# Kernel optimization log

Hardware: AMD Instinct MI355X
Metric: run time of the kernel (lower is better)

The kernel has to match this reference:

```python
import jax, jax.numpy as jnp
import numpy as np

TIMESTEPS = 1000
DIFFUSION_SPEED = 0.01
B, N = 4, 2048
E = N * (N - 1) // 2  # strict lower-triangular entries per graph


def _build_Qt():
    # Qt[t-1] = [[1-f, f], [f, 1-f]],  f = 0.5*(1-(1-2s)^t), t = 1..T
    ts = jnp.arange(1, TIMESTEPS + 1, dtype=jnp.float32)
    flip = 0.5 * (1.0 - (1.0 - 2.0 * DIFFUSION_SPEED) ** ts)          # [T]
    row0 = jnp.stack([1.0 - flip, flip], axis=-1)                      # [T,2]
    row1 = jnp.stack([flip, 1.0 - flip], axis=-1)                      # [T,2]
    return jnp.stack([row0, row1], axis=1)                             # [T,2,2]


def setup_inputs() -> dict:
    key = jax.random.key(0)
    k1, k2, k3, k4 = jax.random.split(key, 4)
    adj_start = jax.random.randint(k1, (B, N, N), 0, 2, dtype=jnp.int32)
    t = jax.random.randint(k2, (B,), 0, TIMESTEPS, dtype=jnp.int32)
    u = jax.random.uniform(k3, (B, N, N), dtype=jnp.float32)
    q_approx = jax.random.normal(k4, (B, E), dtype=jnp.float32)
    return {"adj_start": adj_start, "t": t, "u": u, "q_approx": q_approx}


def reference(adj_start, t, u, q_approx):
    Qt = _build_Qt()                                                   # [T,2,2]
    # symmetrize raw adjacency into a binary undirected adjacency
    a = jnp.tril(adj_start, -1)
    adj0 = a + jnp.swapaxes(a, -1, -2)                                 # [B,N,N] in {0,1}

    b_idx = jnp.arange(B)[:, None, None]

    # ---- forward diffusion: sample x_t ~ Categorical(Qt[t][adj0]) ----
    probs = Qt[t][b_idx, adj0]                                         # [B,N,N,2]
    x_t = (u < probs[..., 1]).astype(adj0.dtype)                       # [B,N,N]

    # ---- backward diffusion: q(x_{t-1} | x_t, x_0) ----
    Q_likelihood = Qt[0]                                               # [2,2]
    Q_prior = Qt[t - 1]                                                # [B,2,2] (t=0 wraps, as in torch)
    Q_evidence = Qt[t]                                                 # [B,2,2]

    likelihood = Q_likelihood[x_t]                                     # [B,N,N,2]
    prior = Q_prior[b_idx, adj0]                                       # [B,N,N,2]
    evidence = Q_evidence[b_idx, adj0, x_t]                            # [B,N,N]
    q_backward = likelihood * prior / evidence[..., None]              # [B,N,N,2]

    ti, tj = np.tril_indices(N, -1)                                    # static indices
    q_target = q_backward[:, ti, tj, 1]                                # [B,E]

    # ---- BCE-with-logits loss (mean) ----
    x = q_approx
    loss = jnp.mean(jnp.maximum(x, 0.0) - x * q_target + jnp.log1p(jnp.exp(-jnp.abs(x))))
    return loss
```

## Files before the change

kernel.cpp:

```cpp
#include <hip/hip_runtime.h>
#include <math.h>

#define TIMESTEPS 1000
constexpr int Bc  = 4;
constexpr int Nc  = 2048;
constexpr int EcI = Nc * (Nc - 1) / 2;
constexpr int EG  = EcI / 4;

constexpr int BLKX    = 128;
constexpr int THREADS = 256;
constexpr int ITERS   = 8;
constexpr int ITERSTRIDE = BLKX * THREADS * 2;

typedef int   i4v __attribute__((ext_vector_type(4)));
typedef float f4v __attribute__((ext_vector_type(4)));

__device__ __forceinline__ int imin(int a, int b) { return a < b ? a : b; }

struct GData { i4v av; f4v uv; f4v qv; };

__device__ __forceinline__ GData issue_group(
    const int* __restrict__ adjb, const float* __restrict__ ub,
    const float* __restrict__ qb, int gc)
{
    GData d;
    const int e0 = gc << 2;
    const float sf = sqrtf((float)(8 * e0 + 1));
    int i = (int)((1.0f + sf) * 0.5f);
    if (i * (i - 1) / 2 > e0)  --i;
    if (i * (i + 1) / 2 <= e0) ++i;
    int jj = e0 - i * (i - 1) / 2;
    d.qv = *(const f4v*)(qb + e0);
    int ii = i;
    #pragma unroll
    for (int k = 0; k < 4; ++k) {
        const bool adv = (jj >= ii);
        ii += adv;
        jj = adv ? 0 : jj;
        const int base = (ii << 11) + jj;
        d.av[k] = adjb[base];
        d.uv[k] = ub[base];
        ++jj;
    }
    return d;
}

__device__ __forceinline__ float group_sum(const GData& d,
    float p0, float p1, float qt00, float qt01, float qt10, float qt11)
{
    float s = 0.0f;
    #pragma unroll
    for (int k = 0; k < 4; ++k) {
        const int   a0 = d.av[k];
        const float ps = a0 ? p1 : p0;
        const bool  x  = d.uv[k] < ps;
        const float t0 = x ? qt01 : qt00;
        const float t1 = x ? qt11 : qt10;
        const float qt = a0 ? t1 : t0;
        const float qq = d.qv[k];
        s += fmaxf(qq, 0.0f) - qq * qt + __logf(1.0f + __expf(-fabsf(qq)));
    }
    return s;
}

__global__ __launch_bounds__(256, 2) void diff_loss_kernel(
    const int* __restrict__ adj, const int* __restrict__ t,
    const float* __restrict__ u, const float* __restrict__ q,
    double* __restrict__ partials)
{
    const int b  = blockIdx.y;
    const int bx = blockIdx.x;
    const int tb = t[b];

    const float f_t   = 0.5f * (1.0f - powf(0.98f, (float)(tb + 1)));
    const int   tpe   = (tb == 0) ? TIMESTEPS : tb;
    const float f_p   = 0.5f * (1.0f - powf(0.98f, (float)tpe));
    const float f0    = 0.01f;
    const float omf_t = 1.0f - f_t;

    const float p0   = f_t;
    const float p1   = omf_t;
    const float qt00 = f0          * f_p          / omf_t;
    const float qt01 = (1.0f - f0) * f_p          / f_t;
    const float qt10 = f0          * (1.0f - f_p) / f_t;
    const float qt11 = (1.0f - f0) * (1.0f - f_p) / omf_t;

    const int*   adjb = adj + ((size_t)b << 22);
    const float* ub   = u   + ((size_t)b << 22);
    const float* qb   = q   + (size_t)b * EcI;

    const int gbase = bx * 512 + threadIdx.x;

    GData A0 = issue_group(adjb, ub, qb, gbase);
    GData B0 = issue_group(adjb, ub, qb, gbase + 256);
    GData A1 = issue_group(adjb, ub, qb, gbase + ITERSTRIDE);
    GData B1 = issue_group(adjb, ub, qb, gbase + ITERSTRIDE + 256);

    double acc = 0.0;

    #pragma unroll 1
    for (int k = 0; k < ITERS; ++k) {
        GData An = A1, Bn = B1;
        if (k + 2 < ITERS) {
            const int gk = gbase + (k + 2) * ITERSTRIDE;
            An = issue_group(adjb, ub, qb, gk);
            Bn = issue_group(adjb, ub, qb, imin(gk + 256, EG - 1));
        }

        const float sA = group_sum(A0, p0, p1, qt00, qt01, qt10, qt11);
        const float sB = group_sum(B0, p0, p1, qt00, qt01, qt10, qt11);
        const int g1 = gbase + k * ITERSTRIDE + 256;
        acc += (double)(sA + ((g1 < EG) ? sB : 0.0f));

        A0 = A1; B0 = B1; A1 = An; B1 = Bn;
    }

    for (int off = 32; off > 0; off >>= 1)
        acc += __shfl_down(acc, off, 64);
    __shared__ double wsum[4];
    const int lane = threadIdx.x & 63, wid = threadIdx.x >> 6;
    if (lane == 0) wsum[wid] = acc;
    __syncthreads();
    if (threadIdx.x == 0)
        partials[blockIdx.y * BLKX + blockIdx.x] =
            wsum[0] + wsum[1] + wsum[2] + wsum[3];
}

__global__ __launch_bounds__(256) void final_reduce_kernel(
    const double* __restrict__ partials, int nb, float* __restrict__ out)
{
    double acc = 0.0;
    for (int idx = threadIdx.x; idx < nb; idx += blockDim.x)
        acc += partials[idx];
    for (int off = 32; off > 0; off >>= 1)
        acc += __shfl_down(acc, off, 64);
    __shared__ double wsum[4];
    const int lane = threadIdx.x & 63, wid = threadIdx.x >> 6;
    if (lane == 0) wsum[wid] = acc;
    __syncthreads();
    if (threadIdx.x == 0)
        out[0] = (float)((wsum[0] + wsum[1] + wsum[2] + wsum[3]) /
                         ((double)Bc * (double)EcI));
}

extern "C" void kernel_launch(void* const* d_in, const int* in_sizes, int n_in,
                              void* d_out, int out_size, void* d_ws, size_t ws_size,
                              hipStream_t stream) {
    const int*   adj = (const int*)d_in[0];
    const int*   t   = (const int*)d_in[1];
    const float* u   = (const float*)d_in[2];
    const float* q   = (const float*)d_in[3];
    float*  out      = (float*)d_out;
    double* partials = (double*)d_ws;

    dim3 grid(BLKX, Bc);
    diff_loss_kernel<<<grid, THREADS, 0, stream>>>(adj, t, u, q, partials);
    final_reduce_kernel<<<1, 256, 0, stream>>>(partials, BLKX * Bc, out);
}
```

Before: 164.8 us.

## Iterate adjacency in row-major chunks with vector loads instead of triangular index mapping

Replaces the per-edge triangular index decoding (sqrt-based row recovery plus four scalar gathers of adj and u) with a grid-stride loop over 4-wide row-major chunks of the full NxN matrix, skipping chunks above the diagonal. adj and u are now read as aligned 16-byte nontemporal vector loads, q is read as an unaligned vector, and the diagonal-straddling chunks are masked. The grid grows to 512 blocks and the prefetch pipeline and launch-bounds occupancy hint are dropped. Half the threads do no work on skipped chunks, and the explicit software prefetching is lost.

```diff
diff --git a/kernel.cpp b/kernel.cpp
--- a/kernel.cpp
+++ b/kernel.cpp
@@ -5,71 +5,23 @@
 constexpr int Bc  = 4;
 constexpr int Nc  = 2048;
 constexpr int EcI = Nc * (Nc - 1) / 2;
-constexpr int EG  = EcI / 4;
+constexpr int CHUNKS = Nc * Nc / 4;
 
-constexpr int BLKX    = 128;
+constexpr int BLKX    = 512;
 constexpr int THREADS = 256;
-constexpr int ITERS   = 8;
-constexpr int ITERSTRIDE = BLKX * THREADS * 2;
 
 typedef int   i4v __attribute__((ext_vector_type(4)));
 typedef float f4v __attribute__((ext_vector_type(4)));
+typedef float f4u __attribute__((ext_vector_type(4), aligned(4)));
 
 __device__ __forceinline__ int imin(int a, int b) { return a < b ? a : b; }
 
-struct GData { i4v av; f4v uv; f4v qv; };
-
-__device__ __forceinline__ GData issue_group(
-    const int* __restrict__ adjb, const float* __restrict__ ub,
-    const float* __restrict__ qb, int gc)
-{
-    GData d;
-    const int e0 = gc << 2;
-    const float sf = sqrtf((float)(8 * e0 + 1));
-    int i = (int)((1.0f + sf) * 0.5f);
-    if (i * (i - 1) / 2 > e0)  --i;
-    if (i * (i + 1) / 2 <= e0) ++i;
-    int jj = e0 - i * (i - 1) / 2;
-    d.qv = *(const f4v*)(qb + e0);
-    int ii = i;
-    #pragma unroll
-    for (int k = 0; k < 4; ++k) {
-        const bool adv = (jj >= ii);
-        ii += adv;
-        jj = adv ? 0 : jj;
-        const int base = (ii << 11) + jj;
-        d.av[k] = adjb[base];
-        d.uv[k] = ub[base];
-        ++jj;
-    }
-    return d;
-}
-
-__device__ __forceinline__ float group_sum(const GData& d,
-    float p0, float p1, float qt00, float qt01, float qt10, float qt11)
-{
-    float s = 0.0f;
-    #pragma unroll
-    for (int k = 0; k < 4; ++k) {
-        const int   a0 = d.av[k];
-        const float ps = a0 ? p1 : p0;
-        const bool  x  = d.uv[k] < ps;
-        const float t0 = x ? qt01 : qt00;
-        const float t1 = x ? qt11 : qt10;
-        const float qt = a0 ? t1 : t0;
-        const float qq = d.qv[k];
-        s += fmaxf(qq, 0.0f) - qq * qt + __logf(1.0f + __expf(-fabsf(qq)));
-    }
-    return s;
-}
-
-__global__ __launch_bounds__(256, 2) void diff_loss_kernel(
+__global__ __launch_bounds__(256) void diff_loss_kernel(
     const int* __restrict__ adj, const int* __restrict__ t,
     const float* __restrict__ u, const float* __restrict__ q,
     double* __restrict__ partials)
 {
     const int b  = blockIdx.y;
-    const int bx = blockIdx.x;
     const int tb = t[b];
 
     const float f_t   = 0.5f * (1.0f - powf(0.98f, (float)(tb + 1)));
@@ -89,30 +41,44 @@
     const float* ub   = u   + ((size_t)b << 22);
     const float* qb   = q   + (size_t)b * EcI;
 
-    const int gbase = bx * 512 + threadIdx.x;
-
-    GData A0 = issue_group(adjb, ub, qb, gbase);
-    GData B0 = issue_group(adjb, ub, qb, gbase + 256);
-    GData A1 = issue_group(adjb, ub, qb, gbase + ITERSTRIDE);
-    GData B1 = issue_group(adjb, ub, qb, gbase + ITERSTRIDE + 256);
-
+    const int stride = BLKX * THREADS;
     double acc = 0.0;
 
-    #pragma unroll 1
-    for (int k = 0; k < ITERS; ++k) {
-        GData An = A1, Bn = B1;
-        if (k + 2 < ITERS) {
-            const int gk = gbase + (k + 2) * ITERSTRIDE;
-            An = issue_group(adjb, ub, qb, gk);
-            Bn = issue_group(adjb, ub, qb, imin(gk + 256, EG - 1));
+    for (int c = blockIdx.x * THREADS + threadIdx.x; c < CHUNKS; c += stride) {
+        const int r  = c >> 9;
+        const int j0 = (c & 511) << 2;
+        if (j0 >= r) continue;
+
+        const int base = (r << 11) + j0;
+        const i4v a4 = __builtin_nontemporal_load((const i4v*)(adjb + base));
+        const f4v u4 = __builtin_nontemporal_load((const f4v*)(ub   + base));
+
+        const int e = ((r * (r - 1)) >> 1) + j0;
+        float qk[4];
+        if (j0 + 4 <= r) {
+            const f4u q4 = __builtin_nontemporal_load((const f4u*)(qb + e));
+            qk[0] = q4.x; qk[1] = q4.y; qk[2] = q4.z; qk[3] = q4.w;
+        } else {
+            #pragma unroll
+            for (int k = 0; k < 4; ++k)
+                qk[k] = __builtin_nontemporal_load(qb + e + imin(k, r - 1 - j0));
         }
 
-        const float sA = group_sum(A0, p0, p1, qt00, qt01, qt10, qt11);
-        const float sB = group_sum(B0, p0, p1, qt00, qt01, qt10, qt11);
-        const int g1 = gbase + k * ITERSTRIDE + 256;
-        acc += (double)(sA + ((g1 < EG) ? sB : 0.0f));
-
-        A0 = A1; B0 = B1; A1 = An; B1 = Bn;
+        float s = 0.0f;
+        #pragma unroll
+        for (int k = 0; k < 4; ++k) {
+            const int   a0 = a4[k];
+            const float ps = a0 ? p1 : p0;
+            const bool  x  = u4[k] < ps;
+            const float t0 = x ? qt01 : qt00;
+            const float t1 = x ? qt11 : qt10;
+            const float qtv = a0 ? t1 : t0;
+            const float qv  = qk[k];
+            const float term = fmaxf(qv, 0.0f) - qv * qtv
+                             + __logf(1.0f + __expf(-fabsf(qv)));
+            s += (j0 + k < r) ? term : 0.0f;
+        }
+        acc += (double)s;
     }
 
     for (int off = 32; off > 0; off >>= 1)
```

New measurement: 156.7 us. 1.05x faster.
